# Kernel optimization log

Hardware: AMD Instinct MI355X
Metric: run time of the kernel (lower is better)

Reference implementation:

```python
import jax, jax.numpy as jnp
import numpy as np

LATENT = 768
HEADS = 12
HEAD_DIM = LATENT // HEADS
FFN = 4 * LATENT


def setup_inputs() -> dict:
    key = jax.random.key(0)
    ks = jax.random.split(key, 16)
    s = 1.0 / np.sqrt(LATENT)
    inp = {
        "x": jax.random.normal(ks[0], (2, 2048, LATENT), dtype=jnp.float32),
        "Wq": jax.random.normal(ks[1], (LATENT, LATENT), dtype=jnp.float32) * s,
        "bq": jnp.zeros((LATENT,), jnp.float32),
        "Wk": jax.random.normal(ks[2], (LATENT, LATENT), dtype=jnp.float32) * s,
        "bk": jnp.zeros((LATENT,), jnp.float32),
        "Wv": jax.random.normal(ks[3], (LATENT, LATENT), dtype=jnp.float32) * s,
        "bv": jnp.zeros((LATENT,), jnp.float32),
        "Wo": jax.random.normal(ks[4], (LATENT, LATENT), dtype=jnp.float32) * s,
        "bo": jnp.zeros((LATENT,), jnp.float32),
        "ln1_g": jnp.ones((LATENT,), jnp.float32),
        "ln1_b": jnp.zeros((LATENT,), jnp.float32),
        "ln2_g": jnp.ones((LATENT,), jnp.float32),
        "ln2_b": jnp.zeros((LATENT,), jnp.float32),
        "W1": jax.random.normal(ks[5], (FFN, LATENT), dtype=jnp.float32) * s,
        "b1": jnp.zeros((FFN,), jnp.float32),
        "W2": jax.random.normal(ks[6], (LATENT, FFN), dtype=jnp.float32) * (1.0 / np.sqrt(FFN)),
        "b2": jnp.zeros((LATENT,), jnp.float32),
    }
    return inp


def _layernorm(x, g, b, eps=1e-5):
    mu = jnp.mean(x, axis=-1, keepdims=True)
    var = jnp.var(x, axis=-1, keepdims=True)
    return (x - mu) * jax.lax.rsqrt(var + eps) * g + b


def reference(x, Wq, bq, Wk, bk, Wv, bv, Wo, bo, ln1_g, ln1_b, ln2_g, ln2_b, W1, b1, W2, b2):
    b, n, d = x.shape
    # torch Linear: y = x @ W.T + bias
    Q = (x @ Wq.T + bq).reshape(b, n, HEADS, HEAD_DIM).transpose(0, 2, 1, 3)
    K = (x @ Wk.T + bk).reshape(b, n, HEADS, HEAD_DIM).transpose(0, 2, 1, 3)
    V = (x @ Wv.T + bv).reshape(b, n, HEADS, HEAD_DIM).transpose(0, 2, 1, 3)
    scores = jnp.einsum("bhqd,bhkd->bhqk", Q, K) / np.sqrt(HEAD_DIM)  # [b,h,n,n]
    weights = jax.nn.softmax(scores, axis=-1)
    attn = jnp.einsum("bhqk,bhkd->bhqd", weights, V)
    attn = attn.transpose(0, 2, 1, 3).reshape(b, n, d)
    attn = attn @ Wo.T + bo
    x = _layernorm(x + attn, ln1_g, ln1_b)
    h = jax.nn.gelu(x @ W1.T + b1, approximate=False)
    ffn = h @ W2.T + b2
    x = _layernorm(x + ffn, ln2_g, ln2_b)
    return x
```

## Files before the change

kernel.cpp:

```cpp
#include <hip/hip_runtime.h>
#include <hip/hip_bf16.h>
#include <cstddef>
#include <cstdint>

typedef __bf16 bf16_t;
typedef bf16_t bf16x8 __attribute__((ext_vector_type(8)));
typedef bf16_t bf16x4 __attribute__((ext_vector_type(4)));
typedef float f32x4 __attribute__((ext_vector_type(4)));

#define LATENT 768
#define FFN_DIM 3072
#define NTOK 4096
#define SEQ 2048
#define HEADS 12
#define HD 64

#define C2F 0.18033688011112042f

__device__ __forceinline__ void gload_lds16(const bf16_t* g, bf16_t* l) {
    __builtin_amdgcn_global_load_lds((const __attribute__((address_space(1))) void*)g,
                                     (__attribute__((address_space(3))) void*)l, 16, 0, 0);
}

#define SW_SRC(lane)  ((((lane) & 3) ^ (((lane) >> 3) & 3)) * 8)
#define SW_RD(quad, l16)  (((quad) ^ (((l16) >> 1) & 3)) * 8)

struct CvtDesc {
    const float* src[7];
    bf16_t* dst[7];
    int n4[7];
    const float* bsrc[3];
    float* bdst;
};

__global__ __launch_bounds__(256) void cvt_f32_bf16(CvtDesc d) {
    int seg = blockIdx.y;
    if (seg == 7) {
        int which = blockIdx.x;
        if (which >= 3) return;
        int t = threadIdx.x;
#pragma unroll
        for (int i = 0; i < 3; ++i)
            d.bdst[which * LATENT + t + i * 256] = d.bsrc[which][t + i * 256];
        return;
    }
    int i = blockIdx.x * 256 + threadIdx.x;
    if (i >= d.n4[seg]) return;
    float4 v = ((const float4*)d.src[seg])[i];
    bf16x4 o;
    o[0] = (bf16_t)v.x; o[1] = (bf16_t)v.y; o[2] = (bf16_t)v.z; o[3] = (bf16_t)v.w;
    *(bf16x4*)&d.dst[seg][(size_t)i * 4] = o;
}

template<int EPI>
__global__ __launch_bounds__(512) void gemm128(const bf16_t* __restrict__ A,
                                               const bf16_t* __restrict__ B,
                                               const float* __restrict__ bias,
                                               void* __restrict__ Cv,
                                               int M, int N, int K) {
    __shared__ __align__(16) bf16_t As[2][128 * 32];
    __shared__ __align__(16) bf16_t Bs[2][128 * 32];
    int t = threadIdx.x;
    int w = t >> 6;
    int lane = t & 63, l16 = lane & 15, quad = lane >> 4;
    int xt = blockIdx.x + blockIdx.y;
    if (xt >= (int)gridDim.x) xt -= gridDim.x;
    int m0 = xt * 128, n0 = blockIdx.y * 128;
    int wm = w & 1, wn = w >> 1;
    int mrow0 = wm * 64, ncol0 = wn * 32;

    f32x4 acc[4][2] = {};

    int srow = lane >> 2;
    int sseg = SW_SRC(lane);
    int qsw  = SW_RD(quad, l16);

    auto stage = [&](int k0, int buf) {
        const bf16_t* Ag = A + (size_t)(m0 + w * 16 + srow) * K + k0 + sseg;
        gload_lds16(Ag, &As[buf][(w * 16) * 32]);
        const bf16_t* Bg = B + (size_t)(n0 + w * 16 + srow) * K + k0 + sseg;
        gload_lds16(Bg, &Bs[buf][(w * 16) * 32]);
    };

    int niter = K / 32;
    stage(0, 0);
    for (int kt = 0; kt < niter; ++kt) {
        __syncthreads();
        int cur = kt & 1;
        if (kt + 1 < niter) stage((kt + 1) * 32, cur ^ 1);

        bf16x8 a[4], b[2];
#pragma unroll
        for (int i = 0; i < 4; ++i)
            a[i] = *(const bf16x8*)&As[cur][(mrow0 + i * 16 + l16) * 32 + qsw];
#pragma unroll
        for (int j = 0; j < 2; ++j)
            b[j] = *(const bf16x8*)&Bs[cur][(ncol0 + j * 16 + l16) * 32 + qsw];
#pragma unroll
        for (int i = 0; i < 4; ++i)
#pragma unroll
            for (int j = 0; j < 2; ++j)
                acc[i][j] = __builtin_amdgcn_mfma_f32_16x16x32_bf16(a[i], b[j], acc[i][j], 0, 0, 0);
    }

    float* Cf = (float*)Cv;
    bf16_t* Cb = (bf16_t*)Cv;
#pragma unroll
    for (int j = 0; j < 2; ++j) {
        int col = n0 + ncol0 + j * 16 + l16;
        float bvv = bias[col];
#pragma unroll
        for (int i = 0; i < 4; ++i) {
            int row0 = m0 + mrow0 + i * 16 + quad * 4;
#pragma unroll
            for (int r = 0; r < 4; ++r) {
                float v = acc[i][j][r] + bvv;
                if (EPI == 2) v = 0.5f * v * (1.0f + erff(v * 0.70710678118654752f));
                if (EPI == 3) { if (col < LATENT) v *= C2F; }
                if (EPI == 0) Cf[(size_t)(row0 + r) * N + col] = v;
                else          Cb[(size_t)(row0 + r) * N + col] = (bf16_t)v;
            }
        }
    }
}

struct SKDst { float* p[4]; };

__global__ __launch_bounds__(512) void gemm128sk(const bf16_t* __restrict__ A,
                                                 const bf16_t* __restrict__ B,
                                                 const float* __restrict__ bias,
                                                 SKDst dst,
                                                 int M, int N, int Ktot) {
    __shared__ __align__(16) bf16_t As[2][128 * 32];
    __shared__ __align__(16) bf16_t Bs[2][128 * 32];
    int t = threadIdx.x;
    int w = t >> 6;
    int lane = t & 63, l16 = lane & 15, quad = lane >> 4;
    int z = blockIdx.z;
    int KS = Ktot >> 2;
    int kbase = z * KS;
    int m0 = blockIdx.x * 128, n0 = blockIdx.y * 128;
    int wm = w & 1, wn = w >> 1;
    int mrow0 = wm * 64, ncol0 = wn * 32;

    f32x4 acc[4][2] = {};

    int srow = lane >> 2;
    int sseg = SW_SRC(lane);
    int qsw  = SW_RD(quad, l16);

    auto stage = [&](int k0, int buf) {
        const bf16_t* Ag = A + (size_t)(m0 + w * 16 + srow) * Ktot + kbase + k0 + sseg;
        gload_lds16(Ag, &As[buf][(w * 16) * 32]);
        const bf16_t* Bg = B + (size_t)(n0 + w * 16 + srow) * Ktot + kbase + k0 + sseg;
        gload_lds16(Bg, &Bs[buf][(w * 16) * 32]);
    };

    int niter = KS / 32;
    stage(0, 0);
    for (int kt = 0; kt < niter; ++kt) {
        __syncthreads();
        int cur = kt & 1;
        if (kt + 1 < niter) stage((kt + 1) * 32, cur ^ 1);

        bf16x8 a[4], b[2];
#pragma unroll
        for (int i = 0; i < 4; ++i)
            a[i] = *(const bf16x8*)&As[cur][(mrow0 + i * 16 + l16) * 32 + qsw];
#pragma unroll
        for (int j = 0; j < 2; ++j)
            b[j] = *(const bf16x8*)&Bs[cur][(ncol0 + j * 16 + l16) * 32 + qsw];
#pragma unroll
        for (int i = 0; i < 4; ++i)
#pragma unroll
            for (int j = 0; j < 2; ++j)
                acc[i][j] = __builtin_amdgcn_mfma_f32_16x16x32_bf16(a[i], b[j], acc[i][j], 0, 0, 0);
    }

    float* Cf = dst.p[z];
#pragma unroll
    for (int j = 0; j < 2; ++j) {
        int col = n0 + ncol0 + j * 16 + l16;
        float bvv = (z == 0) ? bias[col] : 0.f;
#pragma unroll
        for (int i = 0; i < 4; ++i) {
            int row0 = m0 + mrow0 + i * 16 + quad * 4;
#pragma unroll
            for (int r = 0; r < 4; ++r)
                Cf[(size_t)(row0 + r) * N + col] = acc[i][j][r] + bvv;
        }
    }
}

template<int EPI>
__global__ __launch_bounds__(256) void gemm64(const bf16_t* __restrict__ A,
                                              const bf16_t* __restrict__ B,
                                              const float* __restrict__ bias,
                                              void* __restrict__ Cv,
                                              int M, int N, int K) {
    __shared__ __align__(16) bf16_t As[2][64 * 32];
    __shared__ __align__(16) bf16_t Bs[2][64 * 32];
    int t = threadIdx.x;
    int w = t >> 6;
    int lane = t & 63, l16 = lane & 15, quad = lane >> 4;
    int m0 = blockIdx.x * 64, n0 = blockIdx.y * 64;
    int wm = w & 1, wn = w >> 1;

    f32x4 acc[2][2] = {};

    int srow = lane >> 2;
    int sseg = SW_SRC(lane);
    int qsw  = SW_RD(quad, l16);

    auto stage = [&](int k0, int buf) {
        const bf16_t* Ag = A + (size_t)(m0 + w * 16 + srow) * K + k0 + sseg;
        gload_lds16(Ag, &As[buf][(w * 16) * 32]);
        const bf16_t* Bg = B + (size_t)(n0 + w * 16 + srow) * K + k0 + sseg;
        gload_lds16(Bg, &Bs[buf][(w * 16) * 32]);
    };

    int niter = K / 32;
    stage(0, 0);
    for (int kt = 0; kt < niter; ++kt) {
        __syncthreads();
        int cur = kt & 1;
        if (kt + 1 < niter) stage((kt + 1) * 32, cur ^ 1);

        bf16x8 a[2], b[2];
#pragma unroll
        for (int i = 0; i < 2; ++i)
            a[i] = *(const bf16x8*)&As[cur][(wm * 32 + i * 16 + l16) * 32 + qsw];
#pragma unroll
        for (int j = 0; j < 2; ++j)
            b[j] = *(const bf16x8*)&Bs[cur][(wn * 32 + j * 16 + l16) * 32 + qsw];
#pragma unroll
        for (int i = 0; i < 2; ++i)
#pragma unroll
            for (int j = 0; j < 2; ++j)
                acc[i][j] = __builtin_amdgcn_mfma_f32_16x16x32_bf16(a[i], b[j], acc[i][j], 0, 0, 0);
    }

    float* Cf = (float*)Cv;
    bf16_t* Cb = (bf16_t*)Cv;
#pragma unroll
    for (int j = 0; j < 2; ++j) {
        int col = n0 + wn * 32 + j * 16 + l16;
        float bvv = bias[col];
#pragma unroll
        for (int i = 0; i < 2; ++i) {
            int row0 = m0 + wm * 32 + i * 16 + quad * 4;
#pragma unroll
            for (int r = 0; r < 4; ++r) {
                float v = acc[i][j][r] + bvv;
                if (EPI == 2) v = 0.5f * v * (1.0f + erff(v * 0.70710678118654752f));
                if (EPI == 0) Cf[(size_t)(row0 + r) * N + col] = v;
                else          Cb[(size_t)(row0 + r) * N + col] = (bf16_t)v;
            }
        }
    }
}

__global__ __launch_bounds__(256) void v_transpose(const bf16_t* __restrict__ QKV,
                                                   bf16_t* __restrict__ Vt) {
    __shared__ bf16_t Ts[64][68];
    int t = threadIdx.x;
    int bh = blockIdx.y;
    int b = bh / HEADS, h = bh % HEADS;
    int n0 = blockIdx.x * 64;
    size_t rowbase = (size_t)b * SEQ;
    int r = t >> 3, seg = (t & 7) * 8;
#pragma unroll
    for (int i = 0; i < 2; ++i) {
        int rr = r + i * 32;
        *(bf16x8*)&Ts[rr][seg] =
            *(const bf16x8*)&QKV[(rowbase + n0 + rr) * (3 * LATENT) + 2 * LATENT + h * HD + seg];
    }
    __syncthreads();
#pragma unroll
    for (int i = 0; i < 2; ++i) {
        int d = r + i * 32;
        bf16x8 o;
#pragma unroll
        for (int jj = 0; jj < 8; ++jj) o[jj] = Ts[seg + jj][d];
        *(bf16x8*)&Vt[((size_t)bh * HD + d) * SEQ + n0 + seg] = o;
    }
}

__global__ __launch_bounds__(256) void attn_flash(const bf16_t* __restrict__ QKV,
                                                  const bf16_t* __restrict__ Vt,
                                                  float* __restrict__ Op0,
                                                  float* __restrict__ Op1,
                                                  float* __restrict__ vs0,
                                                  float* __restrict__ vs1) {
    __shared__ __align__(16) bf16_t Ks[2][2][64][32];
    __shared__ __align__(16) bf16_t Vts[2][2][64][32];
    __shared__ __align__(16) bf16_t Ps[4][32][72];

    int t = threadIdx.x;
    int w = t >> 6;
    int lane = t & 63, l16 = lane & 15, quad = lane >> 4;
    int bh = blockIdx.x;
    int b = bh / HEADS, h = bh % HEADS;
    int qblk = blockIdx.y * 128;
    int z = blockIdx.z;
    float* Op = z ? Op1 : Op0;
    float* vs = z ? vs1 : vs0;
    size_t rowbase = (size_t)b * SEQ;
    int kbase = z * (SEQ / 2);
    const int LD = 3 * LATENT;
    int qw = qblk + w * 32;

    bf16x8 bq[2][2];
#pragma unroll
    for (int qt = 0; qt < 2; ++qt) {
        const bf16_t* qrow = QKV + (rowbase + qw + qt * 16 + l16) * LD + h * HD;
        bq[qt][0] = *(const bf16x8*)&qrow[quad * 8];
        bq[qt][1] = *(const bf16x8*)&qrow[32 + quad * 8];
    }

    f32x4 acc[2][4] = {};
    float vsum[2] = {};

    int srow = lane >> 2;
    int sseg = SW_SRC(lane);
    int qsw  = SW_RD(quad, l16);

    {
        const bf16_t* kg = QKV + (rowbase + kbase + w * 16 + srow) * LD + LATENT + h * HD + sseg;
        gload_lds16(kg,      &Ks[0][0][w * 16][0]);
        gload_lds16(kg + 32, &Ks[0][1][w * 16][0]);
        const bf16_t* vg = Vt + ((size_t)bh * HD + w * 16 + srow) * SEQ + kbase + sseg;
        gload_lds16(vg,      &Vts[0][0][w * 16][0]);
        gload_lds16(vg + 32, &Vts[0][1][w * 16][0]);
    }

    for (int kt = 0; kt < SEQ / 128; ++kt) {
        __syncthreads();
        int cur = kt & 1;
        if (kt + 1 < SEQ / 128) {
            int nxt = cur ^ 1;
            int koff = kbase + (kt + 1) * 64;
            const bf16_t* kg = QKV + (rowbase + koff + w * 16 + srow) * LD + LATENT + h * HD + sseg;
            gload_lds16(kg,      &Ks[nxt][0][w * 16][0]);
            gload_lds16(kg + 32, &Ks[nxt][1][w * 16][0]);
            const bf16_t* vg = Vt + ((size_t)bh * HD + w * 16 + srow) * SEQ + koff + sseg;
            gload_lds16(vg,      &Vts[nxt][0][w * 16][0]);
            gload_lds16(vg + 32, &Vts[nxt][1][w * 16][0]);
        }

#pragma unroll
        for (int skt = 0; skt < 4; ++skt) {
            bf16x8 ak0 = *(const bf16x8*)&Ks[cur][0][skt * 16 + l16][qsw];
            bf16x8 ak1 = *(const bf16x8*)&Ks[cur][1][skt * 16 + l16][qsw];
#pragma unroll
            for (int qt = 0; qt < 2; ++qt) {
                f32x4 s = {};
                s = __builtin_amdgcn_mfma_f32_16x16x32_bf16(ak0, bq[qt][0], s, 0, 0, 0);
                s = __builtin_amdgcn_mfma_f32_16x16x32_bf16(ak1, bq[qt][1], s, 0, 0, 0);
                bf16x4 pk;
#pragma unroll
                for (int r = 0; r < 4; ++r) {
                    float p = __builtin_amdgcn_exp2f(s[r]);
                    vsum[qt] += p;
                    pk[r] = (bf16_t)p;
                }
                *(bf16x4*)&Ps[w][qt * 16 + l16][skt * 16 + quad * 4] = pk;
            }
        }
        __threadfence_block();

        bf16x8 bv[4][2];
#pragma unroll
        for (int dt = 0; dt < 4; ++dt) {
            bv[dt][0] = *(const bf16x8*)&Vts[cur][0][dt * 16 + l16][qsw];
            bv[dt][1] = *(const bf16x8*)&Vts[cur][1][dt * 16 + l16][qsw];
        }
#pragma unroll
        for (int qt = 0; qt < 2; ++qt) {
#pragma unroll
            for (int kc = 0; kc < 2; ++kc) {
                bf16x8 ap = *(const bf16x8*)&Ps[w][qt * 16 + l16][kc * 32 + quad * 8];
#pragma unroll
                for (int dt = 0; dt < 4; ++dt)
                    acc[qt][dt] = __builtin_amdgcn_mfma_f32_16x16x32_bf16(ap, bv[dt][kc], acc[qt][dt], 0, 0, 0);
            }
        }
    }

#pragma unroll
    for (int qt = 0; qt < 2; ++qt) {
        vsum[qt] += __shfl_xor(vsum[qt], 16, 64);
        vsum[qt] += __shfl_xor(vsum[qt], 32, 64);
        if (quad == 0)
            vs[(rowbase + qw + qt * 16 + l16) * HEADS + h] = vsum[qt];
    }

#pragma unroll
    for (int qt = 0; qt < 2; ++qt)
#pragma unroll
        for (int dt = 0; dt < 4; ++dt)
#pragma unroll
            for (int r = 0; r < 4; ++r) {
                size_t row = rowbase + qw + qt * 16 + quad * 4 + r;
                Op[row * LATENT + h * HD + dt * 16 + l16] = acc[qt][dt][r];
            }
}

__global__ __launch_bounds__(256) void attn_combine(const float* __restrict__ Op0,
                                                    const float* __restrict__ Op1,
                                                    const float* __restrict__ vs0,
                                                    const float* __restrict__ vs1,
                                                    bf16_t* __restrict__ O) {
    int row = blockIdx.x;
    int t = threadIdx.x;
    const float* a = Op0 + (size_t)row * LATENT;
    const float* bb = Op1 + (size_t)row * LATENT;
#pragma unroll
    for (int i = 0; i < 3; ++i) {
        int c = t + i * 256;
        int h = c >> 6;
        float denom = vs0[(size_t)row * HEADS + h] + vs1[(size_t)row * HEADS + h];
        O[(size_t)row * LATENT + c] = (bf16_t)((a[c] + bb[c]) / denom);
    }
}

template<int NADD>
__global__ __launch_bounds__(256) void ln_residual(const float* __restrict__ base,
                                                   const float* __restrict__ a1,
                                                   const float* __restrict__ a2,
                                                   const float* __restrict__ a3,
                                                   const float* __restrict__ a4,
                                                   const float* __restrict__ g,
                                                   const float* __restrict__ bta,
                                                   float* __restrict__ outf,
                                                   bf16_t* __restrict__ outb) {
    int row = blockIdx.x;
    size_t ro = (size_t)row * LATENT;
    int t = threadIdx.x;
    float v[3];
    float s = 0.f;
#pragma unroll
    for (int i = 0; i < 3; ++i) {
        int cix = t + i * 256;
        float x = base[ro + cix] + a1[ro + cix];
        if (NADD >= 2) x += a2[ro + cix];
        if (NADD >= 3) x += a3[ro + cix];
        if (NADD >= 4) x += a4[ro + cix];
        v[i] = x;
        s += x;
    }
    __shared__ float red[4];
#pragma unroll
    for (int off = 1; off < 64; off <<= 1) s += __shfl_xor(s, off, 64);
    if ((t & 63) == 0) red[t >> 6] = s;
    __syncthreads();
    float mu = (red[0] + red[1] + red[2] + red[3]) * (1.f / LATENT);
    float q = 0.f;
#pragma unroll
    for (int i = 0; i < 3; ++i) {
        float d = v[i] - mu;
        q += d * d;
    }
#pragma unroll
    for (int off = 1; off < 64; off <<= 1) q += __shfl_xor(q, off, 64);
    __syncthreads();
    if ((t & 63) == 0) red[t >> 6] = q;
    __syncthreads();
    float var = (red[0] + red[1] + red[2] + red[3]) * (1.f / LATENT);
    float rs = rsqrtf(var + 1e-5f);
#pragma unroll
    for (int i = 0; i < 3; ++i) {
        int cix = t + i * 256;
        float o = (v[i] - mu) * rs * g[cix] + bta[cix];
        outf[ro + cix] = o;
        if (outb) outb[ro + cix] = (bf16_t)o;
    }
}

extern "C" void kernel_launch(void* const* d_in, const int* in_sizes, int n_in,
                              void* d_out, int out_size, void* d_ws, size_t ws_size,
                              hipStream_t stream) {
    const float* x   = (const float*)d_in[0];
    const float* Wq  = (const float*)d_in[1];
    const float* bq  = (const float*)d_in[2];
    const float* Wk  = (const float*)d_in[3];
    const float* bk  = (const float*)d_in[4];
    const float* Wv  = (const float*)d_in[5];
    const float* bv  = (const float*)d_in[6];
    const float* Wo  = (const float*)d_in[7];
    const float* bo  = (const float*)d_in[8];
    const float* g1  = (const float*)d_in[9];
    const float* be1 = (const float*)d_in[10];
    const float* g2  = (const float*)d_in[11];
    const float* be2 = (const float*)d_in[12];
    const float* W1  = (const float*)d_in[13];
    const float* b1  = (const float*)d_in[14];
    const float* W2  = (const float*)d_in[15];
    const float* b2  = (const float*)d_in[16];
    float* out = (float*)d_out;

    char* ws = (char*)d_ws;
    size_t off = 0;
    auto alloc = [&](size_t bytes) {
        char* p = ws + off;
        off = (off + bytes + 255) & ~(size_t)255;
        return p;
    };
    bf16_t* xbf   = (bf16_t*)alloc((size_t)NTOK * LATENT * 2);
    bf16_t* Wcat  = (bf16_t*)alloc((size_t)3 * LATENT * LATENT * 2);
    bf16_t* Wobf  = (bf16_t*)alloc((size_t)LATENT * LATENT * 2);
    bf16_t* W1bf  = (bf16_t*)alloc((size_t)FFN_DIM * LATENT * 2);
    bf16_t* W2bf  = (bf16_t*)alloc((size_t)LATENT * FFN_DIM * 2);
    float*  bcat  = (float*)alloc((size_t)3 * LATENT * 4);
    bf16_t* QKV   = (bf16_t*)alloc((size_t)NTOK * 3 * LATENT * 2);
    bf16_t* attnO = (bf16_t*)alloc((size_t)NTOK * LATENT * 2);
    float*  tmpf  = (float*)alloc((size_t)NTOK * LATENT * 4);
    float*  y1f   = (float*)alloc((size_t)NTOK * LATENT * 4);
    bf16_t* y1bf  = (bf16_t*)alloc((size_t)NTOK * LATENT * 2);
    bf16_t* hbf   = (bf16_t*)alloc((size_t)NTOK * FFN_DIM * 2);
    float*  vsa   = (float*)alloc((size_t)NTOK * HEADS * 4);
    float*  vsb   = (float*)alloc((size_t)NTOK * HEADS * 4);
    float*  P3    = (float*)alloc((size_t)NTOK * LATENT * 4);
    bf16_t* Vtg   = (bf16_t*)hbf;
    float*  Oa    = tmpf;
    float*  Ob    = y1f;
    float* P0 = tmpf;
    float* P1 = (float*)QKV;
    float* P2 = (float*)xbf;

    CvtDesc cd;
    cd.src[0] = x;   cd.dst[0] = xbf;                        cd.n4[0] = NTOK * LATENT / 4;
    cd.src[1] = Wq;  cd.dst[1] = Wcat;                       cd.n4[1] = LATENT * LATENT / 4;
    cd.src[2] = Wk;  cd.dst[2] = Wcat + LATENT * LATENT;     cd.n4[2] = LATENT * LATENT / 4;
    cd.src[3] = Wv;  cd.dst[3] = Wcat + 2 * LATENT * LATENT; cd.n4[3] = LATENT * LATENT / 4;
    cd.src[4] = Wo;  cd.dst[4] = Wobf;                       cd.n4[4] = LATENT * LATENT / 4;
    cd.src[5] = W1;  cd.dst[5] = W1bf;                       cd.n4[5] = FFN_DIM * LATENT / 4;
    cd.src[6] = W2;  cd.dst[6] = W2bf;                       cd.n4[6] = FFN_DIM * LATENT / 4;
    cd.bsrc[0] = bq; cd.bsrc[1] = bk; cd.bsrc[2] = bv;
    cd.bdst = bcat;
    {
        int maxn4 = NTOK * LATENT / 4;
        dim3 grid((maxn4 + 255) / 256, 8);
        cvt_f32_bf16<<<grid, 256, 0, stream>>>(cd);
    }

    gemm128<3><<<dim3(NTOK / 128, 3 * LATENT / 128), 512, 0, stream>>>(
        xbf, Wcat, bcat, QKV, NTOK, 3 * LATENT, LATENT);

    v_transpose<<<dim3(SEQ / 64, 2 * HEADS), 256, 0, stream>>>(QKV, Vtg);

    attn_flash<<<dim3(2 * HEADS, SEQ / 128, 2), 256, 0, stream>>>(QKV, Vtg, Oa, Ob, vsa, vsb);

    attn_combine<<<NTOK, 256, 0, stream>>>(Oa, Ob, vsa, vsb, attnO);

    gemm64<0><<<dim3(NTOK / 64, LATENT / 64), 256, 0, stream>>>(
        attnO, Wobf, bo, tmpf, NTOK, LATENT, LATENT);

    ln_residual<1><<<NTOK, 256, 0, stream>>>(x, tmpf, nullptr, nullptr, nullptr,
                                             g1, be1, y1f, y1bf);

    gemm128<2><<<dim3(NTOK / 128, FFN_DIM / 128), 512, 0, stream>>>(
        y1bf, W1bf, b1, hbf, NTOK, FFN_DIM, LATENT);

    SKDst skd;
    skd.p[0] = P0; skd.p[1] = P1; skd.p[2] = P2; skd.p[3] = P3;
    gemm128sk<<<dim3(NTOK / 128, LATENT / 128, 4), 512, 0, stream>>>(
        hbf, W2bf, b2, skd, NTOK, LATENT, FFN_DIM);

    ln_residual<4><<<NTOK, 256, 0, stream>>>(y1f, P0, P1, P2, P3,
                                             g2, be2, out, nullptr);
}
```

Baseline: 291.6 us.

## Replace split-K attention with single-pass 64-query blocks and fused normalization

The attention kernel no longer splits the key range across two z-blocks that write fp32 partial outputs and row sums for a separate combine kernel. Each block now covers 64 queries (16 per wave) over the full key sequence, normalizes in registers, and writes bf16 output directly. This drops the combine launch and the fp32 partial-output traffic, and keeps the same number of blocks. In exchange each wave does half the query work per K/V tile it loads, so K/V reuse from LDS per MFMA is lower and the loop is twice as long.

```diff
diff --git a/kernel.cpp b/kernel.cpp
--- a/kernel.cpp
+++ b/kernel.cpp
@@ -288,84 +288,67 @@
 
 __global__ __launch_bounds__(256) void attn_flash(const bf16_t* __restrict__ QKV,
                                                   const bf16_t* __restrict__ Vt,
-                                                  float* __restrict__ Op0,
-                                                  float* __restrict__ Op1,
-                                                  float* __restrict__ vs0,
-                                                  float* __restrict__ vs1) {
+                                                  bf16_t* __restrict__ O) {
     __shared__ __align__(16) bf16_t Ks[2][2][64][32];
     __shared__ __align__(16) bf16_t Vts[2][2][64][32];
-    __shared__ __align__(16) bf16_t Ps[4][32][72];
+    __shared__ __align__(16) bf16_t Ps[4][16][72];
 
     int t = threadIdx.x;
     int w = t >> 6;
     int lane = t & 63, l16 = lane & 15, quad = lane >> 4;
     int bh = blockIdx.x;
     int b = bh / HEADS, h = bh % HEADS;
-    int qblk = blockIdx.y * 128;
-    int z = blockIdx.z;
-    float* Op = z ? Op1 : Op0;
-    float* vs = z ? vs1 : vs0;
+    int qblk = blockIdx.y * 64;
     size_t rowbase = (size_t)b * SEQ;
-    int kbase = z * (SEQ / 2);
     const int LD = 3 * LATENT;
-    int qw = qblk + w * 32;
-
-    bf16x8 bq[2][2];
-#pragma unroll
-    for (int qt = 0; qt < 2; ++qt) {
-        const bf16_t* qrow = QKV + (rowbase + qw + qt * 16 + l16) * LD + h * HD;
-        bq[qt][0] = *(const bf16x8*)&qrow[quad * 8];
-        bq[qt][1] = *(const bf16x8*)&qrow[32 + quad * 8];
-    }
-
-    f32x4 acc[2][4] = {};
-    float vsum[2] = {};
+    int qw = qblk + w * 16;
+
+    bf16x8 bq[2];
+    {
+        const bf16_t* qrow = QKV + (rowbase + qw + l16) * LD + h * HD;
+        bq[0] = *(const bf16x8*)&qrow[quad * 8];
+        bq[1] = *(const bf16x8*)&qrow[32 + quad * 8];
+    }
+
+    f32x4 acc[4] = {};
+    float vsum = 0.f;
 
     int srow = lane >> 2;
     int sseg = SW_SRC(lane);
     int qsw  = SW_RD(quad, l16);
 
-    {
-        const bf16_t* kg = QKV + (rowbase + kbase + w * 16 + srow) * LD + LATENT + h * HD + sseg;
-        gload_lds16(kg,      &Ks[0][0][w * 16][0]);
-        gload_lds16(kg + 32, &Ks[0][1][w * 16][0]);
-        const bf16_t* vg = Vt + ((size_t)bh * HD + w * 16 + srow) * SEQ + kbase + sseg;
-        gload_lds16(vg,      &Vts[0][0][w * 16][0]);
-        gload_lds16(vg + 32, &Vts[0][1][w * 16][0]);
-    }
-
-    for (int kt = 0; kt < SEQ / 128; ++kt) {
+    auto stage = [&](int koff, int buf) {
+        const bf16_t* kg = QKV + (rowbase + koff + w * 16 + srow) * LD + LATENT + h * HD + sseg;
+        gload_lds16(kg,      &Ks[buf][0][w * 16][0]);
+        gload_lds16(kg + 32, &Ks[buf][1][w * 16][0]);
+        const bf16_t* vg = Vt + ((size_t)bh * HD + w * 16 + srow) * SEQ + koff + sseg;
+        gload_lds16(vg,      &Vts[buf][0][w * 16][0]);
+        gload_lds16(vg + 32, &Vts[buf][1][w * 16][0]);
+    };
+
+    stage(0, 0);
+
+    const int NKT = SEQ / 64;
+    for (int kt = 0; kt < NKT; ++kt) {
         __syncthreads();
         int cur = kt & 1;
-        if (kt + 1 < SEQ / 128) {
-            int nxt = cur ^ 1;
-            int koff = kbase + (kt + 1) * 64;
-            const bf16_t* kg = QKV + (rowbase + koff + w * 16 + srow) * LD + LATENT + h * HD + sseg;
-            gload_lds16(kg,      &Ks[nxt][0][w * 16][0]);
-            gload_lds16(kg + 32, &Ks[nxt][1][w * 16][0]);
-            const bf16_t* vg = Vt + ((size_t)bh * HD + w * 16 + srow) * SEQ + koff + sseg;
-            gload_lds16(vg,      &Vts[nxt][0][w * 16][0]);
-            gload_lds16(vg + 32, &Vts[nxt][1][w * 16][0]);
-        }
+        if (kt + 1 < NKT) stage((kt + 1) * 64, cur ^ 1);
 
 #pragma unroll
         for (int skt = 0; skt < 4; ++skt) {
             bf16x8 ak0 = *(const bf16x8*)&Ks[cur][0][skt * 16 + l16][qsw];
             bf16x8 ak1 = *(const bf16x8*)&Ks[cur][1][skt * 16 + l16][qsw];
-#pragma unroll
-            for (int qt = 0; qt < 2; ++qt) {
-                f32x4 s = {};
-                s = __builtin_amdgcn_mfma_f32_16x16x32_bf16(ak0, bq[qt][0], s, 0, 0, 0);
-                s = __builtin_amdgcn_mfma_f32_16x16x32_bf16(ak1, bq[qt][1], s, 0, 0, 0);
-                bf16x4 pk;
-#pragma unroll
-                for (int r = 0; r < 4; ++r) {
-                    float p = __builtin_amdgcn_exp2f(s[r]);
-                    vsum[qt] += p;
-                    pk[r] = (bf16_t)p;
-                }
-                *(bf16x4*)&Ps[w][qt * 16 + l16][skt * 16 + quad * 4] = pk;
+            f32x4 s = {};
+            s = __builtin_amdgcn_mfma_f32_16x16x32_bf16(ak0, bq[0], s, 0, 0, 0);
+            s = __builtin_amdgcn_mfma_f32_16x16x32_bf16(ak1, bq[1], s, 0, 0, 0);
+            bf16x4 pk;
+#pragma unroll
+            for (int r = 0; r < 4; ++r) {
+                float p = __builtin_amdgcn_exp2f(s[r]);
+                vsum += p;
+                pk[r] = (bf16_t)p;
             }
+            *(bf16x4*)&Ps[w][l16][skt * 16 + quad * 4] = pk;
         }
         __threadfence_block();
 
@@ -376,52 +359,28 @@
             bv[dt][1] = *(const bf16x8*)&Vts[cur][1][dt * 16 + l16][qsw];
         }
 #pragma unroll
-        for (int qt = 0; qt < 2; ++qt) {
-#pragma unroll
-            for (int kc = 0; kc < 2; ++kc) {
-                bf16x8 ap = *(const bf16x8*)&Ps[w][qt * 16 + l16][kc * 32 + quad * 8];
-#pragma unroll
-                for (int dt = 0; dt < 4; ++dt)
-                    acc[qt][dt] = __builtin_amdgcn_mfma_f32_16x16x32_bf16(ap, bv[dt][kc], acc[qt][dt], 0, 0, 0);
-            }
-        }
-    }
-
-#pragma unroll
-    for (int qt = 0; qt < 2; ++qt) {
-        vsum[qt] += __shfl_xor(vsum[qt], 16, 64);
-        vsum[qt] += __shfl_xor(vsum[qt], 32, 64);
-        if (quad == 0)
-            vs[(rowbase + qw + qt * 16 + l16) * HEADS + h] = vsum[qt];
-    }
-
-#pragma unroll
-    for (int qt = 0; qt < 2; ++qt)
-#pragma unroll
-        for (int dt = 0; dt < 4; ++dt)
-#pragma unroll
-            for (int r = 0; r < 4; ++r) {
-                size_t row = rowbase + qw + qt * 16 + quad * 4 + r;
-                Op[row * LATENT + h * HD + dt * 16 + l16] = acc[qt][dt][r];
-            }
-}
-
-__global__ __launch_bounds__(256) void attn_combine(const float* __restrict__ Op0,
-                                                    const float* __restrict__ Op1,
-                                                    const float* __restrict__ vs0,
-                                                    const float* __restrict__ vs1,
-                                                    bf16_t* __restrict__ O) {
-    int row = blockIdx.x;
-    int t = threadIdx.x;
-    const float* a = Op0 + (size_t)row * LATENT;
-    const float* bb = Op1 + (size_t)row * LATENT;
-#pragma unroll
-    for (int i = 0; i < 3; ++i) {
-        int c = t + i * 256;
-        int h = c >> 6;
-        float denom = vs0[(size_t)row * HEADS + h] + vs1[(size_t)row * HEADS + h];
-        O[(size_t)row * LATENT + c] = (bf16_t)((a[c] + bb[c]) / denom);
-    }
+        for (int kc = 0; kc < 2; ++kc) {
+            bf16x8 ap = *(const bf16x8*)&Ps[w][l16][kc * 32 + quad * 8];
+#pragma unroll
+            for (int dt = 0; dt < 4; ++dt)
+                acc[dt] = __builtin_amdgcn_mfma_f32_16x16x32_bf16(ap, bv[dt][kc], acc[dt], 0, 0, 0);
+        }
+    }
+
+    vsum += __shfl_xor(vsum, 16, 64);
+    vsum += __shfl_xor(vsum, 32, 64);
+    float dv[4];
+#pragma unroll
+    for (int r = 0; r < 4; ++r)
+        dv[r] = __shfl(vsum, quad * 4 + r, 64);
+
+#pragma unroll
+    for (int dt = 0; dt < 4; ++dt)
+#pragma unroll
+        for (int r = 0; r < 4; ++r) {
+            size_t row = rowbase + qw + quad * 4 + r;
+            O[row * LATENT + h * HD + dt * 16 + l16] = (bf16_t)(acc[dt][r] / dv[r]);
+        }
 }
 
 template<int NADD>
@@ -518,12 +477,8 @@
     float*  y1f   = (float*)alloc((size_t)NTOK * LATENT * 4);
     bf16_t* y1bf  = (bf16_t*)alloc((size_t)NTOK * LATENT * 2);
     bf16_t* hbf   = (bf16_t*)alloc((size_t)NTOK * FFN_DIM * 2);
-    float*  vsa   = (float*)alloc((size_t)NTOK * HEADS * 4);
-    float*  vsb   = (float*)alloc((size_t)NTOK * HEADS * 4);
     float*  P3    = (float*)alloc((size_t)NTOK * LATENT * 4);
     bf16_t* Vtg   = (bf16_t*)hbf;
-    float*  Oa    = tmpf;
-    float*  Ob    = y1f;
     float* P0 = tmpf;
     float* P1 = (float*)QKV;
     float* P2 = (float*)xbf;
@@ -549,9 +504,7 @@
 
     v_transpose<<<dim3(SEQ / 64, 2 * HEADS), 256, 0, stream>>>(QKV, Vtg);
 
-    attn_flash<<<dim3(2 * HEADS, SEQ / 128, 2), 256, 0, stream>>>(QKV, Vtg, Oa, Ob, vsa, vsb);
-
-    attn_combine<<<NTOK, 256, 0, stream>>>(Oa, Ob, vsa, vsb, attnO);
+    attn_flash<<<dim3(2 * HEADS, SEQ / 64), 256, 0, stream>>>(QKV, Vtg, attnO);
 
     gemm64<0><<<dim3(NTOK / 64, LATENT / 64), 256, 0, stream>>>(
         attnO, Wobf, bo, tmpf, NTOK, LATENT, LATENT);
```

After: 290.4 us. Within noise of the previous version (-0.4%).
